# Kernel tuning notes

Measured on AMD Instinct MI355X. Metric: run time of the kernel, lower is better.

Reference implementation:

```python
import jax, jax.numpy as jnp
import numpy as np

B, S, E = 4, 1024, 1024
H, DK, HS = 16, 64, 64
FF = 4096
EPS = 1e-6


def _layernorm(x, g, b):
    mu = jnp.mean(x, axis=-1, keepdims=True)
    var = jnp.mean((x - mu) ** 2, axis=-1, keepdims=True)
    return (x - mu) * jax.lax.rsqrt(var + EPS) * g + b


def setup_inputs() -> dict:
    key = jax.random.key(0)
    ks = jax.random.split(key, 20)
    s_e = 1.0 / np.sqrt(E)
    s_ff = 1.0 / np.sqrt(FF)
    d = {
        "x": jax.random.normal(ks[0], (B, S, E), jnp.float32),
        "pos_encoding": jax.random.normal(ks[1], (S, S, 8), jnp.float32),
        # weights stored [in, out] (torch Linear transposed)
        "Wq": jax.random.normal(ks[2], (E, H * DK), jnp.float32) * s_e,
        "bq": jnp.zeros((H * DK,), jnp.float32),
        "Wk": jax.random.normal(ks[3], (E, H * DK), jnp.float32) * s_e,
        "bk": jnp.zeros((H * DK,), jnp.float32),
        "Wv": jax.random.normal(ks[4], (E, H * HS), jnp.float32) * s_e,
        "bv": jnp.zeros((H * HS,), jnp.float32),
        "Wo": jax.random.normal(ks[5], (H * HS, E), jnp.float32) * s_e,
        "bo": jnp.zeros((E,), jnp.float32),
        "Wg": jax.random.normal(ks[6], (E, E), jnp.float32) * s_e,
        "bg": jnp.zeros((E,), jnp.float32),
        "Wf1": jax.random.normal(ks[7], (E, FF), jnp.float32) * s_e,
        "bf1": jnp.zeros((FF,), jnp.float32),
        "Wfg": jax.random.normal(ks[8], (E, FF), jnp.float32) * s_e,
        "bfg": jnp.zeros((FF,), jnp.float32),
        "Wf2": jax.random.normal(ks[9], (FF, E), jnp.float32) * s_ff,
        "bf2": jnp.zeros((E,), jnp.float32),
        "ln1_g": jnp.ones((E,), jnp.float32),
        "ln1_b": jnp.zeros((E,), jnp.float32),
        "ln2_g": jnp.ones((E,), jnp.float32),
        "ln2_b": jnp.zeros((E,), jnp.float32),
    }
    return d


def reference(x, pos_encoding, Wq, bq, Wk, bk, Wv, bv, Wo, bo, Wg, bg,
              Wf1, bf1, Wfg, bfg, Wf2, bf2, ln1_g, ln1_b, ln2_g, ln2_b):
    b, s, _ = x.shape
    q = (x @ Wq + bq).reshape(b, s, H, DK)
    k = (x @ Wk + bk).reshape(b, s, H, DK)
    v = (x @ Wv + bv).reshape(b, s, H, HS)
    scale = jnp.sqrt(jnp.float32(DK))
    # [b, h, q, k]
    scores = jnp.einsum("bqhd,bkhd->bhqk", q, k) / scale
    pos_bias = jnp.mean(pos_encoding[:s, :s, :], axis=-1)  # [s, s]
    scores = scores + pos_bias[None, None, :, :]
    probs = jax.nn.softmax(scores, axis=-1)
    ctx = jnp.einsum("bhqk,bkhd->bqhd", probs, v).reshape(b, s, H * HS)
    attn_out = ctx @ Wo + bo
    attn_out = jax.nn.sigmoid(x @ Wg + bg) * attn_out
    x1 = _layernorm(x + attn_out, ln1_g, ln1_b)
    ff = (x1 @ Wf1 + bf1) * jax.nn.sigmoid(x1 @ Wfg + bfg)
    ff = ff @ Wf2 + bf2
    return _layernorm(x1 + ff, ln2_g, ln2_b)
```

## Files before the change

### kernel.cpp

```cpp
#include <hip/hip_runtime.h>

constexpr int NB = 4, NS = 1024, NE = 1024, NH = 16, NFF = 4096;
constexpr int NM = NB * NS;

typedef short s8v __attribute__((ext_vector_type(8)));
typedef short s4v __attribute__((ext_vector_type(4)));
typedef float f4  __attribute__((ext_vector_type(4)));

__device__ __forceinline__ float b2f(unsigned short u) {
    union { unsigned int i; float f; } v; v.i = ((unsigned int)u) << 16; return v.f;
}
__device__ __forceinline__ unsigned short f2b(float f) {
    union { float f; unsigned int i; } v; v.f = f;
    unsigned int r = v.i + 0x7FFFu + ((v.i >> 16) & 1u);
    return (unsigned short)(r >> 16);
}
__device__ __forceinline__ float sigf(float x) { return 1.f / (1.f + __expf(-x)); }

#define GL2LDS(g, l) __builtin_amdgcn_global_load_lds( \
    (const __attribute__((address_space(1))) void*)(g), \
    (__attribute__((address_space(3))) void*)(l), 16, 0, 0)

__device__ __forceinline__ void cvt_t_tile(
    const float* __restrict__ W, unsigned short* __restrict__ WT,
    int K, int N, int bx, int by, int t, unsigned short L[64][72])
{
    const int k0 = by * 64, n0 = bx * 64;
    const int r = t >> 4, c4 = (t & 15) * 4;
#pragma unroll
    for (int p = 0; p < 4; p++) {
        int k = r + p * 16;
        f4 v = *(const f4*)&W[(size_t)(k0 + k) * N + n0 + c4];
#pragma unroll
        for (int i = 0; i < 4; i++) L[c4 + i][k] = f2b(v[i]);
    }
    __syncthreads();
    const int n = t >> 2, kc = (t & 3) * 16;
    s8v o0, o1;
#pragma unroll
    for (int i = 0; i < 8; i++) { o0[i] = (short)L[n][kc + i]; o1[i] = (short)L[n][kc + 8 + i]; }
    unsigned short* dst = WT + (size_t)(n0 + n) * K + k0 + kc;
    *(s8v*)dst = o0; *(s8v*)(dst + 8) = o1;
}

__global__ __launch_bounds__(256) void prep_kernel(
    const float* __restrict__ x, unsigned short* __restrict__ xb,
    const float* Wq, const float* Wk, const float* Wv, const float* Wg,
    const float* Wo,
    unsigned short* WTq, unsigned short* WoT,
    const float* Wf1, const float* Wfg, const float* Wf2,
    unsigned short* Wf1T, unsigned short* WfgT, unsigned short* Wf2T,
    const float* __restrict__ pe, float* __restrict__ biasP)
{
    __shared__ unsigned short L[64][72];
    const int t = threadIdx.x;
    int bid = blockIdx.x;

    if (bid < 2048) {
        size_t i = ((size_t)bid * 256 + t) * 8;
        f4 v0 = *(const f4*)(x + i), v1 = *(const f4*)(x + i + 4);
        s8v o;
#pragma unroll
        for (int j = 0; j < 4; j++) { o[j] = (short)f2b(v0[j]); o[4 + j] = (short)f2b(v1[j]); }
        *(s8v*)(xb + i) = o;
        return;
    }
    bid -= 2048;
    if (bid < 1280) {
        int z = bid >> 8, rem = bid & 255;
        const float* W = (z == 0) ? Wq : (z == 1) ? Wk : (z == 2) ? Wv : (z == 3) ? Wg : Wo;
        unsigned short* WT = (z == 4) ? WoT : WTq + (size_t)z * 1024 * 1024;
        cvt_t_tile(W, WT, 1024, 1024, rem & 15, rem >> 4, t, L);
        return;
    }
    bid -= 1280;
    if (bid < 2048) {
        int z = bid >> 10, rem = bid & 1023;
        cvt_t_tile(z ? Wfg : Wf1, z ? WfgT : Wf1T, 1024, 4096, rem & 63, rem >> 6, t, L);
        return;
    }
    bid -= 2048;
    if (bid < 1024) {
        cvt_t_tile(Wf2, Wf2T, 4096, 1024, bid & 15, bid >> 4, t, L);
        return;
    }
    bid -= 1024;
    {
        int idx = bid * 256 + t;
        const float* p = pe + (size_t)idx * 8;
        f4 v0 = *(const f4*)p, v1 = *(const f4*)(p + 4);
        float s = 0.f;
#pragma unroll
        for (int i = 0; i < 4; i++) s += v0[i] + v1[i];
        biasP[idx] = (s * 0.125f - 8.0f) * 1.44269504f;
    }
}

#define EPI_QKVG     0
#define EPI_GATE_RES 2
#define EPI_RES      4
#define EPI_BIAS     5

template <int EPI, int TM>
__global__ __launch_bounds__(256) void gemm_bt(
    const unsigned short* __restrict__ A,
    const unsigned short* __restrict__ BT,
    const float* b0p, const float* b1p, const float* b2p, const float* b3p,
    const unsigned short* ex1,
    const unsigned short* ex2,
    unsigned short* C, int M, int N, int K)
{
    constexpr int AR = 32 * TM;
    __shared__ short As0[AR * 32], As1[AR * 32];
    __shared__ short Bs0[128 * 32], Bs1[128 * 32];

    const int tid  = threadIdx.x;
    const int m0   = blockIdx.y * AR;
    const int n0   = blockIdx.x * 128;
    const int lane = tid & 63;
    const int wave = tid >> 6;
    const int wm   = (wave >> 1) * (16 * TM), wn = (wave & 1) * 64;
    const int quad = lane >> 4, lo = lane & 15;
    const int lrow = lane >> 2;
    const int lcol = (((lane & 3) ^ ((lane >> 4) & 3))) * 8;
    const int rcol = ((quad ^ ((lo >> 2) & 3))) * 8;

    f4 acc[TM][4];
#pragma unroll
    for (int i = 0; i < TM; i++)
#pragma unroll
        for (int j = 0; j < 4; j++)
#pragma unroll
            for (int r = 0; r < 4; r++) acc[i][j][r] = 0.f;

    const unsigned short* ga = A  + (size_t)(m0 + wave * (AR / 4) + lrow) * K + lcol;
    const unsigned short* gb = BT + (size_t)(n0 + wave * 32 + lrow) * K + lcol;
    short* lA0  = &As0[(wave * (AR / 4)) * 32];
    short* lA1  = &As1[(wave * (AR / 4)) * 32];
    short* lB00 = &Bs0[(wave * 32) * 32];
    short* lB01 = &Bs0[(wave * 32 + 16) * 32];
    short* lB10 = &Bs1[(wave * 32) * 32];
    short* lB11 = &Bs1[(wave * 32 + 16) * 32];

    for (int k0 = 0; k0 < K; k0 += 64) {
#pragma unroll
        for (int t = 0; t < TM / 2; t++) {
            GL2LDS(ga + k0 +      (size_t)t * 16 * K, lA0 + t * 16 * 32);
            GL2LDS(ga + k0 + 32 + (size_t)t * 16 * K, lA1 + t * 16 * 32);
        }
        GL2LDS(gb + k0,               lB00);
        GL2LDS(gb + k0 + 16 * K,      lB01);
        GL2LDS(gb + k0 + 32,          lB10);
        GL2LDS(gb + k0 + 32 + 16 * K, lB11);
        __syncthreads();

        s8v af[TM], bf[4];
#pragma unroll
        for (int i = 0; i < TM; i++)
            af[i] = *(const s8v*)&As0[(wm + i * 16 + lo) * 32 + rcol];
#pragma unroll
        for (int j = 0; j < 4; j++)
            bf[j] = *(const s8v*)&Bs0[(wn + j * 16 + lo) * 32 + rcol];
#pragma unroll
        for (int i = 0; i < TM; i++)
#pragma unroll
            for (int j = 0; j < 4; j++)
                acc[i][j] = __builtin_amdgcn_mfma_f32_16x16x32_bf16(af[i], bf[j], acc[i][j], 0, 0, 0);
#pragma unroll
        for (int i = 0; i < TM; i++)
            af[i] = *(const s8v*)&As1[(wm + i * 16 + lo) * 32 + rcol];
#pragma unroll
        for (int j = 0; j < 4; j++)
            bf[j] = *(const s8v*)&Bs1[(wn + j * 16 + lo) * 32 + rcol];
#pragma unroll
        for (int i = 0; i < TM; i++)
#pragma unroll
            for (int j = 0; j < 4; j++)
                acc[i][j] = __builtin_amdgcn_mfma_f32_16x16x32_bf16(af[i], bf[j], acc[i][j], 0, 0, 0);
        __syncthreads();
    }

    const float* bp = b0p;
    bool do_sig = false;
    if (EPI == EPI_QKVG) {
        int seg = n0 >> 10;
        bp = (seg == 0) ? b0p : (seg == 1) ? b1p : (seg == 2) ? b2p : b3p;
        do_sig = (n0 >= 3072);
    }

#pragma unroll
    for (int i = 0; i < TM; i++) {
#pragma unroll
        for (int j = 0; j < 4; j++) {
#pragma unroll
            for (int r = 0; r < 4; r++) {
                int gm = m0 + wm + i * 16 + quad * 4 + r;
                int gn = n0 + wn + j * 16 + lo;
                size_t idx = (size_t)gm * N + gn;
                float v = acc[i][j][r] + (EPI == EPI_QKVG ? bp[gn & 1023] : bp[gn]);
                if (EPI == EPI_QKVG)          { if (do_sig) v = sigf(v); }
                else if (EPI == EPI_GATE_RES) v = b2f(ex1[idx]) + b2f(ex2[(size_t)gm * 4096 + gn]) * v;
                else if (EPI == EPI_RES)      v = b2f(ex1[idx]) + v;
                C[idx] = f2b(v);
            }
        }
    }
}

__global__ __launch_bounds__(512, 1) void gemm_ff8(
    const unsigned short* __restrict__ A,
    const unsigned short* __restrict__ B1T,
    const unsigned short* __restrict__ B2T,
    const float* __restrict__ bias1, const float* __restrict__ bias2,
    unsigned short* __restrict__ C)
{
    __shared__ short Lds[8 * 8192];

    const int tid  = threadIdx.x;
    const int ln   = tid & 63, wv = tid >> 6;
    const int wr   = wv >> 1, wc = wv & 1;
    const int quad = ln >> 4, lo = ln & 15;
    const int m0   = blockIdx.y * 256, n0 = blockIdx.x * 128;

    const int rowst = wv * 8 + (ln >> 3);
    const int cosrc = ((ln & 7) ^ (ln >> 3)) * 8;
    short* const ldst0 = &Lds[(wv * 8) * 64];

    f4 accA[4][4], accB[4][4];
#pragma unroll
    for (int i = 0; i < 4; i++)
#pragma unroll
        for (int j = 0; j < 4; j++)
#pragma unroll
            for (int r = 0; r < 4; r++) { accA[i][j][r] = 0.f; accB[i][j][r] = 0.f; }

    auto stage_half = [&](int h) {
        if (h >= 64) return;
        const int tt = h >> 2, kind = h & 3, slot = h & 7;
        const unsigned short* gsrc;
        if (kind == 0)      gsrc = A   + (size_t)(m0 + rowst) * 1024 + tt * 64 + cosrc;
        else if (kind == 1) gsrc = A   + (size_t)(m0 + 128 + rowst) * 1024 + tt * 64 + cosrc;
        else if (kind == 2) gsrc = B1T + (size_t)(n0 + rowst) * 1024 + tt * 64 + cosrc;
        else                gsrc = B2T + (size_t)(n0 + rowst) * 1024 + tt * 64 + cosrc;
        short* ldst = ldst0 + slot * 8192;
        GL2LDS(gsrc,                     ldst);
        GL2LDS(gsrc + (size_t)64 * 1024, ldst + 64 * 64);
    };

    int aoff[2], boff[2];
#pragma unroll
    for (int kh = 0; kh < 2; kh++) {
        const int sw = (((kh * 4 + quad) ^ (lo & 7)) * 8);
        aoff[kh] = (((wr & 1) * 64 + lo) * 64) + sw;
        boff[kh] = ((wc * 64 + lo) * 64) + sw;
    }
    const int slA = wr >> 1;

#pragma unroll
    for (int h = 0; h < 5; h++) stage_half(h);
    asm volatile("s_waitcnt vmcnt(2)" ::: "memory");
    __builtin_amdgcn_s_barrier();

    for (int t = 0; t < 16; t++) {
        const int p4 = (t & 1) * 4;
        const short* LA  = &Lds[(p4 + slA) * 8192];
        const short* LB1 = &Lds[(p4 + 2) * 8192];
        const short* LB2 = &Lds[(p4 + 3) * 8192];
        const int hb = 4 * t;
        s8v af[4], bf[4];

#pragma unroll
        for (int i = 0; i < 4; i++) af[i] = *(const s8v*)&LA[aoff[0] + i * 1024];
#pragma unroll
        for (int j = 0; j < 4; j++) bf[j] = *(const s8v*)&LB1[boff[0] + j * 1024];
        stage_half(hb + 5);
        __builtin_amdgcn_s_barrier();
        __builtin_amdgcn_s_setprio(1);
#pragma unroll
        for (int i = 0; i < 4; i++)
#pragma unroll
            for (int j = 0; j < 4; j++)
                accA[i][j] = __builtin_amdgcn_mfma_f32_16x16x32_bf16(af[i], bf[j], accA[i][j], 0, 0, 0);
        __builtin_amdgcn_s_setprio(0);
        __builtin_amdgcn_s_barrier();

#pragma unroll
        for (int j = 0; j < 4; j++) bf[j] = *(const s8v*)&LB2[boff[0] + j * 1024];
        stage_half(hb + 6);
        __builtin_amdgcn_s_barrier();
        __builtin_amdgcn_s_setprio(1);
#pragma unroll
        for (int i = 0; i < 4; i++)
#pragma unroll
            for (int j = 0; j < 4; j++)
                accB[i][j] = __builtin_amdgcn_mfma_f32_16x16x32_bf16(af[i], bf[j], accB[i][j], 0, 0, 0);
        __builtin_amdgcn_s_setprio(0);
        __builtin_amdgcn_s_barrier();

#pragma unroll
        for (int i = 0; i < 4; i++) af[i] = *(const s8v*)&LA[aoff[1] + i * 1024];
#pragma unroll
        for (int j = 0; j < 4; j++) bf[j] = *(const s8v*)&LB1[boff[1] + j * 1024];
        stage_half(hb + 7);
        __builtin_amdgcn_s_barrier();
        __builtin_amdgcn_s_setprio(1);
#pragma unroll
        for (int i = 0; i < 4; i++)
#pragma unroll
            for (int j = 0; j < 4; j++)
                accA[i][j] = __builtin_amdgcn_mfma_f32_16x16x32_bf16(af[i], bf[j], accA[i][j], 0, 0, 0);
        __builtin_amdgcn_s_setprio(0);
        __builtin_amdgcn_s_barrier();

#pragma unroll
        for (int j = 0; j < 4; j++) bf[j] = *(const s8v*)&LB2[boff[1] + j * 1024];
        stage_half(hb + 8);
        __builtin_amdgcn_s_barrier();
        __builtin_amdgcn_s_setprio(1);
#pragma unroll
        for (int i = 0; i < 4; i++)
#pragma unroll
            for (int j = 0; j < 4; j++)
                accB[i][j] = __builtin_amdgcn_mfma_f32_16x16x32_bf16(af[i], bf[j], accB[i][j], 0, 0, 0);
        __builtin_amdgcn_s_setprio(0);
        if (t < 14)       { asm volatile("s_waitcnt vmcnt(2)" ::: "memory"); }
        else if (t == 14) { asm volatile("s_waitcnt vmcnt(0)" ::: "memory"); }
        __builtin_amdgcn_s_barrier();
    }

#pragma unroll
    for (int i = 0; i < 4; i++) {
#pragma unroll
        for (int j = 0; j < 4; j++) {
#pragma unroll
            for (int r = 0; r < 4; r++) {
                int gm = m0 + wr * 64 + i * 16 + quad * 4 + r;
                int gn = n0 + wc * 64 + j * 16 + lo;
                float a = accA[i][j][r] + bias1[gn];
                float g = accB[i][j][r] + bias2[gn];
                C[(size_t)gm * 4096 + gn] = f2b(a * sigf(g));
            }
        }
    }
}

__global__ __launch_bounds__(256) void attn_kernel(
    const unsigned short* __restrict__ QKVG, const float* __restrict__ bias,
    unsigned short* __restrict__ ctx)
{
    __shared__ short Ks[32 * 72];
    __shared__ short Vt[64 * 48];
    __shared__ short Ps[4][16 * 40];

    const int tid = threadIdx.x;
    const int lane = tid & 63, wave = tid >> 6;
    const int quad = lane >> 4, lo = lane & 15;
    const int bh = blockIdx.y;
    const int b = bh >> 4, h = bh & 15;
    const int q0 = blockIdx.x * 64 + wave * 16;
    const size_t base  = (size_t)b * NS * 4096 + (size_t)h * 64;
    const size_t baseK = base + 1024, baseV = base + 2048;
    constexpr float c1 = 0.125f * 1.44269504f;

    s8v aq0 = *(const s8v*)(QKVG + base + (size_t)(q0 + lo) * 4096 + quad * 8);
    s8v aq1 = *(const s8v*)(QKVG + base + (size_t)(q0 + lo) * 4096 + 32 + quad * 8);

    f4 accO[4];
    float l_r[4];
#pragma unroll
    for (int r = 0; r < 4; r++) {
        l_r[r] = 0.f;
#pragma unroll
        for (int j = 0; j < 4; j++) accO[j][r] = 0.f;
    }

    const int skv = tid >> 3, sd8 = (tid & 7) * 8;
    const int vkv = tid & 31, vd8 = (tid >> 5) * 8;
    const int pvk = 2 * (vkv & 15) + (vkv >> 4);

    s8v kk = *(const s8v*)(QKVG + baseK + (size_t)skv * 4096 + sd8);
    s8v vv = *(const s8v*)(QKVG + baseV + (size_t)vkv * 4096 + vd8);

    for (int kv0 = 0; kv0 < NS; kv0 += 32) {
        *(s8v*)&Ks[skv * 72 + sd8] = kk;
#pragma unroll
        for (int i = 0; i < 8; i++) Vt[(vd8 + i) * 48 + pvk] = (short)vv[i];
        __syncthreads();

        s8v kkn = kk, vvn = vv;
        if (kv0 + 32 < NS) {
            kkn = *(const s8v*)(QKVG + baseK + (size_t)(kv0 + 32 + skv) * 4096 + sd8);
            vvn = *(const s8v*)(QKVG + baseV + (size_t)(kv0 + 32 + vkv) * 4096 + vd8);
        }

        f4 sc[2];
#pragma unroll
        for (int cb = 0; cb < 2; cb++) {
            s8v bk0 = *(const s8v*)&Ks[(cb * 16 + lo) * 72 + quad * 8];
            s8v bk1 = *(const s8v*)&Ks[(cb * 16 + lo) * 72 + 32 + quad * 8];
            f4 z;
#pragma unroll
            for (int r = 0; r < 4; r++) z[r] = 0.f;
            z = __builtin_amdgcn_mfma_f32_16x16x32_bf16(aq0, bk0, z, 0, 0, 0);
            sc[cb] = __builtin_amdgcn_mfma_f32_16x16x32_bf16(aq1, bk1, z, 0, 0, 0);
        }

        int* PsI = (int*)&Ps[wave][0];
#pragma unroll
        for (int r = 0; r < 4; r++) {
            int qrow = q0 + quad * 4 + r;
            const float* bp = &bias[(size_t)qrow * NS + kv0];
            float p0 = exp2f(sc[0][r] * c1 + bp[lo]);
            float p1 = exp2f(sc[1][r] * c1 + bp[16 + lo]);
            l_r[r] += p0 + p1;
            unsigned int pk = (unsigned int)f2b(p0) | ((unsigned int)f2b(p1) << 16);
            PsI[(quad * 4 + r) * 20 + lo] = (int)pk;
        }
        s8v pf = *(const s8v*)&Ps[wave][lo * 40 + quad * 8];
#pragma unroll
        for (int j = 0; j < 4; j++) {
            s8v bv = *(const s8v*)&Vt[(j * 16 + lo) * 48 + quad * 8];
            accO[j] = __builtin_amdgcn_mfma_f32_16x16x32_bf16(pf, bv, accO[j], 0, 0, 0);
        }
        __syncthreads();
        kk = kkn; vv = vvn;
    }

#pragma unroll
    for (int r = 0; r < 4; r++) {
        float l = l_r[r];
#pragma unroll
        for (int d = 1; d < 16; d <<= 1) l += __shfl_xor(l, d, 64);
        l_r[r] = 1.f / l;
    }
#pragma unroll
    for (int j = 0; j < 4; j++)
#pragma unroll
        for (int r = 0; r < 4; r++) {
            int qrow = q0 + quad * 4 + r;
            ctx[((size_t)b * NS + qrow) * 1024 + h * 64 + j * 16 + lo] = f2b(accO[j][r] * l_r[r]);
        }
}

__global__ __launch_bounds__(256) void ln_kernel(
    const unsigned short* __restrict__ X, const float* __restrict__ g,
    const float* __restrict__ bb, void* __restrict__ out, int outF32)
{
    const int row = blockIdx.x;
    const unsigned short* xr = X + (size_t)row * NE;
    s4v xv = *(const s4v*)(xr + threadIdx.x * 4);
    float v[4], s = 0.f, ss = 0.f;
#pragma unroll
    for (int i = 0; i < 4; i++) {
        v[i] = b2f((unsigned short)xv[i]);
        s += v[i]; ss += v[i] * v[i];
    }
#pragma unroll
    for (int d = 1; d < 64; d <<= 1) { s += __shfl_xor(s, d, 64); ss += __shfl_xor(ss, d, 64); }
    __shared__ float red[8];
    int wave = threadIdx.x >> 6, lane = threadIdx.x & 63;
    if (lane == 0) { red[wave] = s; red[4 + wave] = ss; }
    __syncthreads();
    s  = red[0] + red[1] + red[2] + red[3];
    ss = red[4] + red[5] + red[6] + red[7];
    float mu = s * (1.f / NE);
    float var = ss * (1.f / NE) - mu * mu;
    float rstd = rsqrtf(fmaxf(var, 0.f) + 1e-6f);
#pragma unroll
    for (int i = 0; i < 4; i++) {
        int c = threadIdx.x * 4 + i;
        size_t idx = (size_t)row * NE + c;
        float o = (v[i] - mu) * rstd * g[c] + bb[c];
        if (outF32) ((float*)out)[idx] = o;
        else        ((unsigned short*)out)[idx] = f2b(o);
    }
}

extern "C" void kernel_launch(void* const* d_in, const int* in_sizes, int n_in,
                              void* d_out, int out_size, void* d_ws, size_t ws_size,
                              hipStream_t stream)
{
    const float* x    = (const float*)d_in[0];
    const float* pe   = (const float*)d_in[1];
    const float* Wq   = (const float*)d_in[2];
    const float* bq   = (const float*)d_in[3];
    const float* Wk   = (const float*)d_in[4];
    const float* bk   = (const float*)d_in[5];
    const float* Wv   = (const float*)d_in[6];
    const float* bv   = (const float*)d_in[7];
    const float* Wo   = (const float*)d_in[8];
    const float* bo   = (const float*)d_in[9];
    const float* Wg   = (const float*)d_in[10];
    const float* bg   = (const float*)d_in[11];
    const float* Wf1  = (const float*)d_in[12];
    const float* bf1  = (const float*)d_in[13];
    const float* Wfg  = (const float*)d_in[14];
    const float* bfg  = (const float*)d_in[15];
    const float* Wf2  = (const float*)d_in[16];
    const float* bf2  = (const float*)d_in[17];
    const float* ln1g = (const float*)d_in[18];
    const float* ln1b = (const float*)d_in[19];
    const float* ln2g = (const float*)d_in[20];
    const float* ln2b = (const float*)d_in[21];

    char* ws = (char*)d_ws;
    unsigned short* xb    = (unsigned short*)ws;
    unsigned short* WTq   = (unsigned short*)(ws + ( 8ull << 20));
    unsigned short* WoT   = (unsigned short*)(ws + (16ull << 20));
    unsigned short* Wf1T  = (unsigned short*)(ws + (18ull << 20));
    unsigned short* WfgT  = (unsigned short*)(ws + (26ull << 20));
    unsigned short* Wf2T  = (unsigned short*)(ws + (34ull << 20));
    float*          biasP = (float*)(ws + (42ull << 20));
    unsigned short* QKVG  = (unsigned short*)(ws + (46ull << 20));
    unsigned short* T1 = xb;
    unsigned short* Cx = WTq;
    unsigned short* X1 = WTq;
    unsigned short* H1 = QKVG;
    unsigned short* T2 = xb;

    dim3 blk(256);

    prep_kernel<<<dim3(2048 + 1280 + 2048 + 1024 + 4096), blk, 0, stream>>>(
        x, xb, Wq, Wk, Wv, Wg, Wo, WTq, WoT,
        Wf1, Wfg, Wf2, Wf1T, WfgT, Wf2T, pe, biasP);

    gemm_bt<EPI_QKVG, 4><<<dim3(32, 32), blk, 0, stream>>>(
        xb, WTq, bq, bk, bv, bg, nullptr, nullptr, QKVG, NM, 4096, NE);

    attn_kernel<<<dim3(NS / 64, NB * NH), blk, 0, stream>>>(QKVG, biasP, Cx);

    gemm_bt<EPI_GATE_RES, 2><<<dim3(8, 64), blk, 0, stream>>>(
        Cx, WoT, bo, nullptr, nullptr, nullptr, xb, QKVG + 3072, T1, NM, NE, NE);
    ln_kernel<<<dim3(NM), blk, 0, stream>>>(T1, ln1g, ln1b, X1, 0);

    gemm_ff8<<<dim3(NFF / 128, NM / 256), dim3(512), 0, stream>>>(
        X1, Wf1T, WfgT, bf1, bfg, H1);

    gemm_bt<EPI_RES, 2><<<dim3(8, 64), blk, 0, stream>>>(
        H1, Wf2T, bf2, nullptr, nullptr, nullptr, X1, nullptr, T2, NM, NE, NFF);
    ln_kernel<<<dim3(NM), blk, 0, stream>>>(T2, ln2g, ln2b, d_out, 1);
}
```

Measured before the change: 472.1 us.

## Route QKVG GEMM through dual-B 8-wave kernel and split-K the FF2 GEMM

The QKVG projection now uses the 512-thread dual-accumulator kernel, which loads each A tile once and multiplies it against two 128-column B slices, so each block covers 256 output columns. The FF2 GEMM (K=4096) becomes a two-way split-K 8-wave kernel that writes fp32 partials into workspace and into the output buffer. A new LayerNorm kernel adds the two partials, the bias and the residual before normalising. This aims to raise MFMA efficiency and occupancy for the narrow-N FF2 GEMM. In exchange it adds extra fp32 partial-sum traffic.

```diff
diff --git a/kernel.cpp b/kernel.cpp
--- a/kernel.cpp
+++ b/kernel.cpp
@@ -96,18 +96,14 @@
     }
 }
 
-#define EPI_QKVG     0
 #define EPI_GATE_RES 2
-#define EPI_RES      4
-#define EPI_BIAS     5
 
 template <int EPI, int TM>
 __global__ __launch_bounds__(256) void gemm_bt(
     const unsigned short* __restrict__ A,
     const unsigned short* __restrict__ BT,
-    const float* b0p, const float* b1p, const float* b2p, const float* b3p,
-    const unsigned short* ex1,
-    const unsigned short* ex2,
+    const float* b0p,
+    const unsigned short* ex1, const unsigned short* ex2,
     unsigned short* C, int M, int N, int K)
 {
     constexpr int AR = 32 * TM;
@@ -180,14 +176,6 @@
         __syncthreads();
     }
 
-    const float* bp = b0p;
-    bool do_sig = false;
-    if (EPI == EPI_QKVG) {
-        int seg = n0 >> 10;
-        bp = (seg == 0) ? b0p : (seg == 1) ? b1p : (seg == 2) ? b2p : b3p;
-        do_sig = (n0 >= 3072);
-    }
-
 #pragma unroll
     for (int i = 0; i < TM; i++) {
 #pragma unroll
@@ -197,21 +185,23 @@
                 int gm = m0 + wm + i * 16 + quad * 4 + r;
                 int gn = n0 + wn + j * 16 + lo;
                 size_t idx = (size_t)gm * N + gn;
-                float v = acc[i][j][r] + (EPI == EPI_QKVG ? bp[gn & 1023] : bp[gn]);
-                if (EPI == EPI_QKVG)          { if (do_sig) v = sigf(v); }
-                else if (EPI == EPI_GATE_RES) v = b2f(ex1[idx]) + b2f(ex2[(size_t)gm * 4096 + gn]) * v;
-                else if (EPI == EPI_RES)      v = b2f(ex1[idx]) + v;
+                float v = acc[i][j][r] + b0p[gn];
+                v = b2f(ex1[idx]) + b2f(ex2[(size_t)gm * 4096 + gn]) * v;
                 C[idx] = f2b(v);
             }
         }
     }
 }
 
-__global__ __launch_bounds__(512, 1) void gemm_ff8(
+#define EPI_FF   0
+#define EPI_QKVG 1
+
+template <int EPI, int NMUL>
+__global__ __launch_bounds__(512, 1) void gemm_dual8(
     const unsigned short* __restrict__ A,
     const unsigned short* __restrict__ B1T,
     const unsigned short* __restrict__ B2T,
-    const float* __restrict__ bias1, const float* __restrict__ bias2,
+    const float* b0, const float* b1, const float* b2, const float* b3,
     unsigned short* __restrict__ C)
 {
     __shared__ short Lds[8 * 8192];
@@ -220,7 +210,7 @@
     const int ln   = tid & 63, wv = tid >> 6;
     const int wr   = wv >> 1, wc = wv & 1;
     const int quad = ln >> 4, lo = ln & 15;
-    const int m0   = blockIdx.y * 256, n0 = blockIdx.x * 128;
+    const int m0   = blockIdx.y * 256, n0 = blockIdx.x * NMUL;
 
     const int rowst = wv * 8 + (ln >> 3);
     const int cosrc = ((ln & 7) ^ (ln >> 3)) * 8;
@@ -328,6 +318,13 @@
         __builtin_amdgcn_s_barrier();
     }
 
+    const float* bp = b0;
+    bool do_sig = false;
+    if (EPI == EPI_QKVG) {
+        int seg = n0 >> 10;
+        bp = (seg == 0) ? b0 : (seg == 1) ? b1 : (seg == 2) ? b2 : b3;
+        do_sig = (n0 >= 3072);
+    }
 #pragma unroll
     for (int i = 0; i < 4; i++) {
 #pragma unroll
@@ -336,9 +333,128 @@
             for (int r = 0; r < 4; r++) {
                 int gm = m0 + wr * 64 + i * 16 + quad * 4 + r;
                 int gn = n0 + wc * 64 + j * 16 + lo;
-                float a = accA[i][j][r] + bias1[gn];
-                float g = accB[i][j][r] + bias2[gn];
-                C[(size_t)gm * 4096 + gn] = f2b(a * sigf(g));
+                if (EPI == EPI_FF) {
+                    float a = accA[i][j][r] + b0[gn];
+                    float g = accB[i][j][r] + b1[gn];
+                    C[(size_t)gm * 4096 + gn] = f2b(a * sigf(g));
+                } else {
+                    float vA = accA[i][j][r] + bp[gn & 1023];
+                    int gnB = gn + 128;
+                    float vB = accB[i][j][r] + bp[gnB & 1023];
+                    if (do_sig) { vA = sigf(vA); vB = sigf(vB); }
+                    C[(size_t)gm * 4096 + gn]  = f2b(vA);
+                    C[(size_t)gm * 4096 + gnB] = f2b(vB);
+                }
+            }
+        }
+    }
+}
+
+__global__ __launch_bounds__(512, 1) void gemm_sk8(
+    const unsigned short* __restrict__ A,
+    const unsigned short* __restrict__ BT,
+    float* __restrict__ P0, float* __restrict__ P1)
+{
+    constexpr int NT = 32;
+    __shared__ short Lds[6 * 8192];
+
+    const int tid  = threadIdx.x;
+    const int ln   = tid & 63, wv = tid >> 6;
+    const int wr   = wv >> 1, wc = wv & 1;
+    const int quad = ln >> 4, lo = ln & 15;
+    const int m0   = blockIdx.y * 256, n0 = blockIdx.x * 128;
+    const int kb   = blockIdx.z * 2048;
+    float* const P = blockIdx.z ? P1 : P0;
+
+    const int rowst = wv * 8 + (ln >> 3);
+    const int cosrc = ((ln & 7) ^ (ln >> 3)) * 8;
+    short* const ldst0 = &Lds[(wv * 8) * 64];
+
+    f4 acc[4][4];
+#pragma unroll
+    for (int i = 0; i < 4; i++)
+#pragma unroll
+        for (int j = 0; j < 4; j++)
+#pragma unroll
+            for (int r = 0; r < 4; r++) acc[i][j][r] = 0.f;
+
+    auto stage_half = [&](int h) {
+        if (h >= 3 * NT) return;
+        const int tt = h / 3, kind = h % 3, slot = h % 6;
+        const unsigned short* gsrc;
+        if (kind == 0)      gsrc = A  + (size_t)(m0 + rowst) * 4096 + kb + tt * 64 + cosrc;
+        else if (kind == 1) gsrc = A  + (size_t)(m0 + 128 + rowst) * 4096 + kb + tt * 64 + cosrc;
+        else                gsrc = BT + (size_t)(n0 + rowst) * 4096 + kb + tt * 64 + cosrc;
+        short* ldst = ldst0 + slot * 8192;
+        GL2LDS(gsrc,                     ldst);
+        GL2LDS(gsrc + (size_t)64 * 4096, ldst + 64 * 64);
+    };
+
+    int aoff[2], boff[2];
+#pragma unroll
+    for (int kh = 0; kh < 2; kh++) {
+        const int sw = (((kh * 4 + quad) ^ (lo & 7)) * 8);
+        aoff[kh] = (((wr & 1) * 64 + lo) * 64) + sw;
+        boff[kh] = ((wc * 64 + lo) * 64) + sw;
+    }
+    const int slA = wr >> 1;
+
+#pragma unroll
+    for (int h = 0; h < 4; h++) stage_half(h);
+    asm volatile("s_waitcnt vmcnt(2)" ::: "memory");
+    __builtin_amdgcn_s_barrier();
+
+    for (int t = 0; t < NT; t++) {
+        const int base = (t & 1) * 3;
+        const short* LA = &Lds[(base + slA) * 8192];
+        const short* LB = &Lds[(base + 2) * 8192];
+        s8v af[4], bf[4];
+
+#pragma unroll
+        for (int i = 0; i < 4; i++) af[i] = *(const s8v*)&LA[aoff[0] + i * 1024];
+#pragma unroll
+        for (int j = 0; j < 4; j++) bf[j] = *(const s8v*)&LB[boff[0] + j * 1024];
+        stage_half(3 * t + 4);
+        __builtin_amdgcn_s_barrier();
+        __builtin_amdgcn_s_setprio(1);
+#pragma unroll
+        for (int i = 0; i < 4; i++)
+#pragma unroll
+            for (int j = 0; j < 4; j++)
+                acc[i][j] = __builtin_amdgcn_mfma_f32_16x16x32_bf16(af[i], bf[j], acc[i][j], 0, 0, 0);
+        __builtin_amdgcn_s_setprio(0);
+        __builtin_amdgcn_s_barrier();
+
+#pragma unroll
+        for (int i = 0; i < 4; i++) af[i] = *(const s8v*)&LA[aoff[1] + i * 1024];
+#pragma unroll
+        for (int j = 0; j < 4; j++) bf[j] = *(const s8v*)&LB[boff[1] + j * 1024];
+        stage_half(3 * t + 5);
+        __builtin_amdgcn_s_barrier();
+        __builtin_amdgcn_s_setprio(1);
+#pragma unroll
+        for (int i = 0; i < 4; i++)
+#pragma unroll
+            for (int j = 0; j < 4; j++)
+                acc[i][j] = __builtin_amdgcn_mfma_f32_16x16x32_bf16(af[i], bf[j], acc[i][j], 0, 0, 0);
+        __builtin_amdgcn_s_setprio(0);
+        __builtin_amdgcn_s_barrier();
+
+        stage_half(3 * t + 6);
+        if (t < NT - 2)       { asm volatile("s_waitcnt vmcnt(2)" ::: "memory"); }
+        else if (t == NT - 2) { asm volatile("s_waitcnt vmcnt(0)" ::: "memory"); }
+        __builtin_amdgcn_s_barrier();
+    }
+
+#pragma unroll
+    for (int i = 0; i < 4; i++) {
+#pragma unroll
+        for (int j = 0; j < 4; j++) {
+#pragma unroll
+            for (int r = 0; r < 4; r++) {
+                int gm = m0 + wr * 64 + i * 16 + quad * 4 + r;
+                int gn = n0 + wc * 64 + j * 16 + lo;
+                P[(size_t)gm * 1024 + gn] = acc[i][j][r];
             }
         }
     }
@@ -444,7 +560,7 @@
 
 __global__ __launch_bounds__(256) void ln_kernel(
     const unsigned short* __restrict__ X, const float* __restrict__ g,
-    const float* __restrict__ bb, void* __restrict__ out, int outF32)
+    const float* __restrict__ bb, unsigned short* __restrict__ out)
 {
     const int row = blockIdx.x;
     const unsigned short* xr = X + (size_t)row * NE;
@@ -469,10 +585,45 @@
 #pragma unroll
     for (int i = 0; i < 4; i++) {
         int c = threadIdx.x * 4 + i;
-        size_t idx = (size_t)row * NE + c;
         float o = (v[i] - mu) * rstd * g[c] + bb[c];
-        if (outF32) ((float*)out)[idx] = o;
-        else        ((unsigned short*)out)[idx] = f2b(o);
+        out[(size_t)row * NE + c] = f2b(o);
+    }
+}
+
+__global__ __launch_bounds__(256) void ln2red_kernel(
+    const unsigned short* __restrict__ X1,
+    const float* __restrict__ P0, const float* __restrict__ P1,
+    const float* __restrict__ bf2,
+    const float* __restrict__ g, const float* __restrict__ bb,
+    float* __restrict__ out)
+{
+    const int row = blockIdx.x;
+    const size_t rb = (size_t)row * NE;
+    s4v xv = *(const s4v*)(X1 + rb + threadIdx.x * 4);
+    f4 p0 = *(const f4*)(P0 + rb + threadIdx.x * 4);
+    f4 p1 = *(const f4*)(P1 + rb + threadIdx.x * 4);
+    float v[4], s = 0.f, ss = 0.f;
+#pragma unroll
+    for (int i = 0; i < 4; i++) {
+        int c = threadIdx.x * 4 + i;
+        v[i] = b2f((unsigned short)xv[i]) + p0[i] + p1[i] + bf2[c];
+        s += v[i]; ss += v[i] * v[i];
+    }
+#pragma unroll
+    for (int d = 1; d < 64; d <<= 1) { s += __shfl_xor(s, d, 64); ss += __shfl_xor(ss, d, 64); }
+    __shared__ float red[8];
+    int wave = threadIdx.x >> 6, lane = threadIdx.x & 63;
+    if (lane == 0) { red[wave] = s; red[4 + wave] = ss; }
+    __syncthreads();
+    s  = red[0] + red[1] + red[2] + red[3];
+    ss = red[4] + red[5] + red[6] + red[7];
+    float mu = s * (1.f / NE);
+    float var = ss * (1.f / NE) - mu * mu;
+    float rstd = rsqrtf(fmaxf(var, 0.f) + 1e-6f);
+#pragma unroll
+    for (int i = 0; i < 4; i++) {
+        int c = threadIdx.x * 4 + i;
+        out[rb + c] = (v[i] - mu) * rstd * g[c] + bb[c];
     }
 }
 
@@ -516,7 +667,8 @@
     unsigned short* Cx = WTq;
     unsigned short* X1 = WTq;
     unsigned short* H1 = QKVG;
-    unsigned short* T2 = xb;
+    float* P0 = (float*)(ws + (18ull << 20));
+    float* P1 = (float*)d_out;
 
     dim3 blk(256);
 
@@ -524,19 +676,20 @@
         x, xb, Wq, Wk, Wv, Wg, Wo, WTq, WoT,
         Wf1, Wfg, Wf2, Wf1T, WfgT, Wf2T, pe, biasP);
 
-    gemm_bt<EPI_QKVG, 4><<<dim3(32, 32), blk, 0, stream>>>(
-        xb, WTq, bq, bk, bv, bg, nullptr, nullptr, QKVG, NM, 4096, NE);
+    gemm_dual8<EPI_QKVG, 256><<<dim3(16, 16), dim3(512), 0, stream>>>(
+        xb, WTq, WTq + 128 * 1024, bq, bk, bv, bg, QKVG);
 
     attn_kernel<<<dim3(NS / 64, NB * NH), blk, 0, stream>>>(QKVG, biasP, Cx);
 
     gemm_bt<EPI_GATE_RES, 2><<<dim3(8, 64), blk, 0, stream>>>(
-        Cx, WoT, bo, nullptr, nullptr, nullptr, xb, QKVG + 3072, T1, NM, NE, NE);
-    ln_kernel<<<dim3(NM), blk, 0, stream>>>(T1, ln1g, ln1b, X1, 0);
-
-    gemm_ff8<<<dim3(NFF / 128, NM / 256), dim3(512), 0, stream>>>(
-        X1, Wf1T, WfgT, bf1, bfg, H1);
-
-    gemm_bt<EPI_RES, 2><<<dim3(8, 64), blk, 0, stream>>>(
-        H1, Wf2T, bf2, nullptr, nullptr, nullptr, X1, nullptr, T2, NM, NE, NFF);
-    ln_kernel<<<dim3(NM), blk, 0, stream>>>(T2, ln2g, ln2b, d_out, 1);
-}
+        Cx, WoT, bo, xb, QKVG + 3072, T1, NM, NE, NE);
+    ln_kernel<<<dim3(NM), blk, 0, stream>>>(T1, ln1g, ln1b, X1);
+
+    gemm_dual8<EPI_FF, 128><<<dim3(NFF / 128, NM / 256), dim3(512), 0, stream>>>(
+        X1, Wf1T, WfgT, bf1, bfg, nullptr, nullptr, H1);
+
+    gemm_sk8<<<dim3(8, 16, 2), dim3(512), 0, stream>>>(H1, Wf2T, P0, P1);
+
+    ln2red_kernel<<<dim3(NM), blk, 0, stream>>>(
+        X1, P0, P1, bf2, ln2g, ln2b, (float*)d_out);
+}
```

Result: faster. 428.6 us (-9.2%).
